# Performance work log

Hardware: AMD Instinct MI355X
Metric: run time of the kernel (lower is better)

Reference implementation:

```python
import jax, jax.numpy as jnp
import numpy as np

TH, TW = 64, 64        # template_size (image shape)
OH, OW = 256, 256      # out_size
K = 3                  # spline order
PAD = 4                # hardcoded padding in module
OFF = PAD - (K + 1) // 2          # = 2
CX_OFF = (OH - TH) // 2           # centering_offset[0] = 96
CY_OFF = (OW - TW) // 2           # centering_offset[1] = 96
BATCH = 1024


def bspline3(p):
    # fast cubic B-spline basis, p: (B,) -> (B, 4)
    return jnp.stack([
        p ** 3 / 6,
        -p ** 3 / 2 + p ** 2 / 2 + p / 2 + 1.0 / 6,
        p ** 3 / 2 - p ** 2 + 2.0 / 3,
        (1 - p) ** 3 / 6,
    ], axis=-1)


def setup_inputs() -> dict:
    key = jax.random.key(0)
    k1, k2, k3 = jax.random.split(key, 3)
    coeffs = jax.random.normal(k1, (TH + 2 * PAD, TW + 2 * PAD), jnp.float32)
    x = (jax.random.normal(k2, (BATCH, 1, 1, 1), jnp.float32) - 0.5) * 10
    y = (jax.random.normal(k3, (BATCH, 1, 1, 1), jnp.float32) - 0.5) * 10
    return {"coeffs": coeffs, "x": x, "y": y}


def reference(coeffs, x, y):
    B = x.shape[0]
    # integer pixel shift (floor) and subpixel remainder
    px = jnp.floor(x[:, 0, 0, 0]).astype(jnp.int32)  # (B,)
    py = jnp.floor(y[:, 0, 0, 0]).astype(jnp.int32)  # (B,)
    sx = jnp.remainder(x[:, 0, 0, 0], 1.0)           # (B,)
    sy = jnp.remainder(y[:, 0, 0, 0], 1.0)           # (B,)

    bx = bspline3(sx)  # (B,4) basis along rows (i index)
    by = bspline3(sy)  # (B,4) basis along cols (j index)

    # (4,4,TH+1,TW+1) shifted coefficient windows
    slices = jnp.stack([
        jnp.stack([coeffs[i + OFF:i + OFF + TH + 1, j + OFF:j + OFF + TW + 1]
                   for j in range(K + 1)])
        for i in range(K + 1)])
    # blended template: (B, TH+1, TW+1)
    template = jnp.einsum('bi,bj,ijrc->brc', bx, by, slices)

    bi = jnp.arange(B)[:, None, None]

    # scatter along columns (dim 3 in torch): x_a[b, r, idx_a] = template[b, r, c]
    col = jnp.arange(TW + 1)
    idx_a = jnp.clip(col[None, None, :] + py[:, None, None] + CY_OFF + 1, 0, OW + 1)  # (B,1,TW+1)
    ri = jnp.arange(TH + 1)[None, :, None]
    x_a = jnp.zeros((B, OH + 2, OW + 2), template.dtype)
    x_a = x_a.at[bi, ri, idx_a].set(template)

    # scatter along rows (dim 2 in torch): x_b[b, idx_b, c] = x_a[b, r, c]
    row = jnp.arange(OH + 2)
    idx_b = jnp.clip(row[None, :, None] + px[:, None, None] + CX_OFF + 1, 0, OH + 1)  # (B,OH+2,1)
    ci = jnp.arange(OW + 2)[None, None, :]
    x_b = jnp.zeros_like(x_a).at[bi, idx_b, ci].set(x_a)

    return x_b[:, 1:-1, 1:-1][:, None]  # (B,1,OH,OW)
```

## Files before the change

### kernel.cpp

```cpp
#include <hip/hip_runtime.h>


#define TH 64
#define TW 64
#define CW 72
#define NBLK_PER_IMG 64

__global__ __launch_bounds__(256) void spline2d_kernel(
    const float* __restrict__ coeffs,
    const float* __restrict__ x,
    const float* __restrict__ y,
    float* __restrict__ out)
{
    const int gid = blockIdx.x * 256 + threadIdx.x;
    const int b   = gid >> 14;
    const int rem = gid & 16383;
    const int R   = rem >> 6;
    const int C0  = (rem & 63) << 2;

    const float xv = x[b];
    const float yv = y[b];
    const float fx = floorf(xv), fy = floorf(yv);
    const int   px = (int)fx,    py = (int)fy;
    const float sx = xv - fx,    sy = yv - fy;

    const int r = R - px - 96;

    float4 o = make_float4(0.f, 0.f, 0.f, 0.f);

    if (r >= 0 && r <= TH) {
        float wx0, wx1, wx2, wx3, wy0, wy1, wy2, wy3;
        {
            const float p = sx, p2 = p * p, p3 = p2 * p, q = 1.0f - p;
            wx0 = p3 * (1.0f / 6.0f);
            wx1 = -0.5f * p3 + 0.5f * p2 + 0.5f * p + (1.0f / 6.0f);
            wx2 = 0.5f * p3 - p2 + (2.0f / 3.0f);
            wx3 = q * q * q * (1.0f / 6.0f);
        }
        {
            const float p = sy, p2 = p * p, p3 = p2 * p, q = 1.0f - p;
            wy0 = p3 * (1.0f / 6.0f);
            wy1 = -0.5f * p3 + 0.5f * p2 + 0.5f * p + (1.0f / 6.0f);
            wy2 = 0.5f * p3 - p2 + (2.0f / 3.0f);
            wy3 = q * q * q * (1.0f / 6.0f);
        }

        const int cbase = C0 - py - 96;
        float vals[4];
#pragma unroll
        for (int e = 0; e < 4; ++e) {
            const int c = cbase + e;
            float v = 0.0f;
            if (c >= 0 && c <= TW) {
                const float* p0 = coeffs + (r + 2) * CW + (c + 2);
#pragma unroll
                for (int i = 0; i < 4; ++i) {
                    const float* row = p0 + i * CW;
                    const float s = row[0] * wy0 + row[1] * wy1 +
                                    row[2] * wy2 + row[3] * wy3;
                    v = fmaf((i == 0 ? wx0 : i == 1 ? wx1 : i == 2 ? wx2 : wx3), s, v);
                }
            }
            vals[e] = v;
        }
        o = make_float4(vals[0], vals[1], vals[2], vals[3]);
    }

    reinterpret_cast<float4*>(out)[gid] = o;
}

extern "C" void kernel_launch(void* const* d_in, const int* in_sizes, int n_in,
                              void* d_out, int out_size, void* d_ws, size_t ws_size,
                              hipStream_t stream) {
    const float* coeffs = (const float*)d_in[0];
    const float* x      = (const float*)d_in[1];
    const float* y      = (const float*)d_in[2];
    float* out = (float*)d_out;

    const int nblocks = (out_size / 4 + 255) / 256;
    spline2d_kernel<<<nblocks, 256, 0, stream>>>(coeffs, x, y, out);
}
```

Before: 290.6 us.

## Zero output with memset and compute only the shifted template patch per image

The kernel no longer computes every output pixel. The launcher first clears the whole output with hipMemsetAsync, then runs one block per image that evaluates only the 65x65 patch where the template lands and scatters it with bounds checks. This removes the per-pixel index math and branching over the mostly-zero output. In exchange it adds a second pass over memory, the patch stores are scalar and unaligned, and there is only one block per image.

```diff
diff --git a/kernel.cpp b/kernel.cpp
--- a/kernel.cpp
+++ b/kernel.cpp
@@ -1,22 +1,17 @@
 #include <hip/hip_runtime.h>
 
 
-#define TH 64
-#define TW 64
 #define CW 72
-#define NBLK_PER_IMG 64
+#define PATCH 65
+#define PATCH_ELEMS (PATCH * PATCH)
 
-__global__ __launch_bounds__(256) void spline2d_kernel(
+__global__ __launch_bounds__(256) void spline2d_patch(
     const float* __restrict__ coeffs,
     const float* __restrict__ x,
     const float* __restrict__ y,
     float* __restrict__ out)
 {
-    const int gid = blockIdx.x * 256 + threadIdx.x;
-    const int b   = gid >> 14;
-    const int rem = gid & 16383;
-    const int R   = rem >> 6;
-    const int C0  = (rem & 63) << 2;
+    const int b = blockIdx.x;
 
     const float xv = x[b];
     const float yv = y[b];
@@ -24,49 +19,44 @@
     const int   px = (int)fx,    py = (int)fy;
     const float sx = xv - fx,    sy = yv - fy;
 
-    const int r = R - px - 96;
-
-    float4 o = make_float4(0.f, 0.f, 0.f, 0.f);
-
-    if (r >= 0 && r <= TH) {
-        float wx0, wx1, wx2, wx3, wy0, wy1, wy2, wy3;
-        {
-            const float p = sx, p2 = p * p, p3 = p2 * p, q = 1.0f - p;
-            wx0 = p3 * (1.0f / 6.0f);
-            wx1 = -0.5f * p3 + 0.5f * p2 + 0.5f * p + (1.0f / 6.0f);
-            wx2 = 0.5f * p3 - p2 + (2.0f / 3.0f);
-            wx3 = q * q * q * (1.0f / 6.0f);
-        }
-        {
-            const float p = sy, p2 = p * p, p3 = p2 * p, q = 1.0f - p;
-            wy0 = p3 * (1.0f / 6.0f);
-            wy1 = -0.5f * p3 + 0.5f * p2 + 0.5f * p + (1.0f / 6.0f);
-            wy2 = 0.5f * p3 - p2 + (2.0f / 3.0f);
-            wy3 = q * q * q * (1.0f / 6.0f);
-        }
-
-        const int cbase = C0 - py - 96;
-        float vals[4];
-#pragma unroll
-        for (int e = 0; e < 4; ++e) {
-            const int c = cbase + e;
-            float v = 0.0f;
-            if (c >= 0 && c <= TW) {
-                const float* p0 = coeffs + (r + 2) * CW + (c + 2);
-#pragma unroll
-                for (int i = 0; i < 4; ++i) {
-                    const float* row = p0 + i * CW;
-                    const float s = row[0] * wy0 + row[1] * wy1 +
-                                    row[2] * wy2 + row[3] * wy3;
-                    v = fmaf((i == 0 ? wx0 : i == 1 ? wx1 : i == 2 ? wx2 : wx3), s, v);
-                }
-            }
-            vals[e] = v;
-        }
-        o = make_float4(vals[0], vals[1], vals[2], vals[3]);
+    float wx[4], wy[4];
+    {
+        const float p = sx, p2 = p * p, p3 = p2 * p, q = 1.0f - p;
+        wx[0] = p3 * (1.0f / 6.0f);
+        wx[1] = -0.5f * p3 + 0.5f * p2 + 0.5f * p + (1.0f / 6.0f);
+        wx[2] = 0.5f * p3 - p2 + (2.0f / 3.0f);
+        wx[3] = q * q * q * (1.0f / 6.0f);
+    }
+    {
+        const float p = sy, p2 = p * p, p3 = p2 * p, q = 1.0f - p;
+        wy[0] = p3 * (1.0f / 6.0f);
+        wy[1] = -0.5f * p3 + 0.5f * p2 + 0.5f * p + (1.0f / 6.0f);
+        wy[2] = 0.5f * p3 - p2 + (2.0f / 3.0f);
+        wy[3] = q * q * q * (1.0f / 6.0f);
     }
 
-    reinterpret_cast<float4*>(out)[gid] = o;
+    const int R0 = px + 96;
+    const int C0 = py + 96;
+    float* __restrict__ ob = out + (size_t)b * 65536;
+
+    for (int e = threadIdx.x; e < PATCH_ELEMS; e += 256) {
+        const int r = e / PATCH;
+        const int c = e - r * PATCH;
+        const int R = R0 + r;
+        const int C = C0 + c;
+        if ((unsigned)R < 256u && (unsigned)C < 256u) {
+            const float* p0 = coeffs + (r + 2) * CW + (c + 2);
+            float v = 0.0f;
+#pragma unroll
+            for (int i = 0; i < 4; ++i) {
+                const float* row = p0 + i * CW;
+                const float s = row[0] * wy[0] + row[1] * wy[1] +
+                                row[2] * wy[2] + row[3] * wy[3];
+                v = fmaf(wx[i], s, v);
+            }
+            ob[R * 256 + C] = v;
+        }
+    }
 }
 
 extern "C" void kernel_launch(void* const* d_in, const int* in_sizes, int n_in,
@@ -77,6 +67,8 @@
     const float* y      = (const float*)d_in[2];
     float* out = (float*)d_out;
 
-    const int nblocks = (out_size / 4 + 255) / 256;
-    spline2d_kernel<<<nblocks, 256, 0, stream>>>(coeffs, x, y, out);
+    hipMemsetAsync(out, 0, (size_t)out_size * sizeof(float), stream);
+
+    const int batch = in_sizes[1];
+    spline2d_patch<<<batch, 256, 0, stream>>>(coeffs, x, y, out);
 }
```

Measured after the change: 268.3 us. -7.7%, faster.
